# Kernel tuning notes

Measured on AMD Instinct MI355X. Metric: run time of the kernel, lower is better.

Reference implementation:

```python
import jax, jax.numpy as jnp
import numpy as np

B, C, H, W = 512, 1, 280, 280
K, S, F = 28, 28, 10           # kernel, stride, nfilters
HS, WS = 10, 10                # output spatial spans (280/28)
SPAN = HS * WS                 # 100 patch locations
OUT = 10                       # out_channels
DEC_IN = HS * WS * F           # 1000


def setup_inputs() -> dict:
    key = jax.random.key(0)
    k1, k2, k3, k4, k5 = jax.random.split(key, 5)
    x = jax.random.normal(k1, (B, C, H, W), dtype=jnp.float32)
    # locally-connected weights: one kernel per (filter, spatial location), torch layout [F*SPAN, C, K, K]
    conv_w = jax.random.normal(k2, (F * SPAN, C, K, K), dtype=jnp.float32) * 0.02
    conv_b = jax.random.normal(k3, (F * SPAN, C), dtype=jnp.float32) * 0.02
    dec_w = jax.random.normal(k4, (OUT, DEC_IN), dtype=jnp.float32) * 0.02
    dec_b = jax.random.normal(k5, (OUT,), dtype=jnp.float32) * 0.02
    return {"x": x, "conv_w": conv_w, "conv_b": conv_b, "dec_w": dec_w, "dec_b": dec_b}


def reference(x, conv_w, conv_b, dec_w, dec_b):
    # Extract non-overlapping KxK patches (stride == kernel_size, padding == 0):
    # [B,C,H,W] -> [B,C,HS,K,WS,K] -> [B,HS,WS,C,K,K] -> [B,SPAN,C,K,K]
    # matches torch unfold(2).unfold(3) ordering (height span outer, width span inner).
    patches = x.reshape(B, C, HS, K, WS, K).transpose(0, 2, 4, 1, 3, 5)
    patches = patches.reshape(B, SPAN, C, K, K)
    # weight index in torch is f*SPAN + s (x is tiled SPAN-fastest by repeat)
    w = conv_w.reshape(F, SPAN, C, K, K)
    # per-location elementwise mul + reduce over (kh, kw) == batched tiny contraction
    out = jnp.einsum('bscij,fscij->bfsc', patches, w)  # [B,F,SPAN,C]
    out = out + conv_b.reshape(F, SPAN, C)
    out = out.reshape(B, F, HS, WS)  # valid since C == 1 (as in torch view)
    out = jax.nn.relu(out).reshape(B, DEC_IN)
    return out @ dec_w.T + dec_b
```

## Files before the change

### kernel.cpp

```cpp
#include <hip/hip_runtime.h>

#define HW      280
#define IMG     78400
#define KK      28
#define F_N     10
#define SPAN    100
#define OUT_N   10
#define NB      4
#define RQR     7
#define WQ      (RQR * 7)
#define P_PLANE 512000

__device__ __forceinline__ float red8(float v) {
  v += __int_as_float(__builtin_amdgcn_mov_dpp(__float_as_int(v), 0xB1,  0xF, 0xF, true));
  v += __int_as_float(__builtin_amdgcn_mov_dpp(__float_as_int(v), 0x4E,  0xF, 0xF, true));
  v += __int_as_float(__builtin_amdgcn_mov_dpp(__float_as_int(v), 0x141, 0xF, 0xF, true));
  return v;
}

__global__ __launch_bounds__(256, 4) void lcn_conv(
    const float* __restrict__ x, const float* __restrict__ cw,
    float* __restrict__ P) {
  const int bid = blockIdx.x;
  const int xcd = bid & 7;
  const int idx = bid >> 3;
  const int ws  = idx % 10;
  const int u   = xcd * 20 + idx / 10;
  const int hs  = u % 10;
  const int t   = u / 10;
  const int rq  = t >> 2;
  const int bg  = t & 3;
  const int s   = hs * 10 + ws;

  const int lane = threadIdx.x & 63;
  const int wid  = threadIdx.x >> 6;
  const int c4   = lane & 7;
  const int g    = lane >> 3;
  const int b0   = bg * 128 + wid * 32 + g * 4;

  __shared__ float4 wl[F_N * WQ];
  {
    const float4* wg = reinterpret_cast<const float4*>(cw);
    for (int i = (int)threadIdx.x; i < F_N * WQ; i += 256) {
      const int f = i / WQ, rem = i - f * WQ;
      wl[i] = wg[(f * SPAN + s) * 196 + rq * WQ + rem];
    }
  }
  __syncthreads();

  float acc[NB][F_N];
#pragma unroll
  for (int bi = 0; bi < NB; ++bi)
#pragma unroll
    for (int f = 0; f < F_N; ++f) acc[bi][f] = 0.f;

  const float* xb = x + (size_t)(hs * KK + rq * RQR) * HW + ws * KK + c4 * 4;

#define LOADROW(SLOT, ROW)                                                \
  _Pragma("unroll")                                                       \
  for (int bi = 0; bi < NB; ++bi)                                         \
    xv[SLOT][bi] = *reinterpret_cast<const float4*>(                      \
        xb + (size_t)(b0 + bi) * IMG + (size_t)(ROW) * HW);

#define COMPUTE(ROW, SLOT)                                                \
  {                                                                       \
    _Pragma("unroll")                                                     \
    for (int f = 0; f < F_N; ++f) {                                       \
      const float4 wv = wl[f * WQ + (ROW) * 7 + c4];                      \
      _Pragma("unroll")                                                   \
      for (int bi = 0; bi < NB; ++bi) {                                   \
        acc[bi][f] = fmaf(xv[SLOT][bi].x, wv.x, acc[bi][f]);              \
        acc[bi][f] = fmaf(xv[SLOT][bi].y, wv.y, acc[bi][f]);              \
        acc[bi][f] = fmaf(xv[SLOT][bi].z, wv.z, acc[bi][f]);              \
        acc[bi][f] = fmaf(xv[SLOT][bi].w, wv.w, acc[bi][f]);              \
      }                                                                   \
    }                                                                     \
  }

  if (c4 < 7) {
    float4 xv[3][NB];
    LOADROW(0, 0)
    LOADROW(1, 1)
#pragma unroll
    for (int r = 0; r < RQR; ++r) {
      const int slot = r % 3;
      if (r + 2 < RQR) { const int ns = (r + 2) % 3; LOADROW(ns, r + 2) }
      COMPUTE(r, slot)
    }
  }

#pragma unroll
  for (int bi = 0; bi < NB; ++bi)
#pragma unroll
    for (int f = 0; f < F_N; ++f) acc[bi][f] = red8(acc[bi][f]);

  float* Pp = P + (size_t)rq * P_PLANE + (size_t)s * 512 + b0;
#pragma unroll
  for (int f = 0; f < F_N; ++f) {
    if (c4 == f || c4 == f - 8) {
      float4 v4 = make_float4(acc[0][f], acc[1][f], acc[2][f], acc[3][f]);
      *reinterpret_cast<float4*>(&Pp[(size_t)f * (SPAN * 512)]) = v4;
    }
  }
}

__global__ __launch_bounds__(256) void lcn_dec(
    const float* __restrict__ P, const float* __restrict__ cb,
    const float* __restrict__ dw, float* __restrict__ yp) {
  const int bid    = blockIdx.x;
  const int dchunk = bid >> 3;
  const int bg     = bid & 7;
  const int lane   = threadIdx.x & 63;
  const int swid   = __builtin_amdgcn_readfirstlane((int)(threadIdx.x >> 6));
  const int d0     = dchunk * 40 + swid * 10;

  const float* Pb = P + (size_t)bg * 64 + lane;
  float acc[OUT_N];
#pragma unroll
  for (int o = 0; o < OUT_N; ++o) acc[o] = 0.f;

#pragma unroll
  for (int dd = 0; dd < 10; ++dd) {
    const int d = d0 + dd;
    const float* pd = Pb + (size_t)d * 512;
    const float p = pd[0] + pd[P_PLANE] + pd[2 * (size_t)P_PLANE] + pd[3 * (size_t)P_PLANE];
    const float h = fmaxf(p + cb[d], 0.f);
#pragma unroll
    for (int o = 0; o < OUT_N; ++o)
      acc[o] = fmaf(h, dw[o * 1000 + d], acc[o]);
  }
  float* ypp = yp + (size_t)(dchunk * 4 + swid) * 5120 + bg * 64 + lane;
#pragma unroll
  for (int o = 0; o < OUT_N; ++o) ypp[(size_t)o * 512] = acc[o];
}

__global__ __launch_bounds__(256) void lcn_yred(
    const float* __restrict__ yp, const float* __restrict__ db,
    float* __restrict__ y) {
  const int idx = blockIdx.x * 256 + (int)threadIdx.x;
  const int o = idx >> 9;
  const int b = idx & 511;
  float a = db[o];
#pragma unroll 10
  for (int p = 0; p < 100; ++p) a += yp[(size_t)p * 5120 + idx];
  y[b * OUT_N + o] = a;
}

extern "C" void kernel_launch(void* const* d_in, const int* in_sizes, int n_in,
                              void* d_out, int out_size, void* d_ws, size_t ws_size,
                              hipStream_t stream) {
  const float* x  = (const float*)d_in[0];
  const float* cw = (const float*)d_in[1];
  const float* cb = (const float*)d_in[2];
  const float* dw = (const float*)d_in[3];
  const float* db = (const float*)d_in[4];
  float* y = (float*)d_out;

  float* P  = (float*)d_ws;
  float* yp = P + 4 * (size_t)P_PLANE;

  lcn_conv<<<dim3(1600), dim3(256), 0, stream>>>(x, cw, P);
  lcn_dec <<<dim3(200),  dim3(256), 0, stream>>>(P, cb, dw, yp);
  lcn_yred<<<dim3(20),   dim3(256), 0, stream>>>(yp, db, y);
}
```

Before: 45.56 us.

## Rewrite locally-connected conv with bf16 MFMA and LDS double-buffered input rows

Adds a weight-prep kernel that converts conv weights to bf16 in a padded per-row layout. The conv kernel becomes bf16 MFMA 16x16x32 tiles over 16-image batch groups. Input rows are staged through swizzled, double-buffered LDS, with prefetching of the next row overlapped with the MFMAs. This replaces scalar FP32 FMAs and the DPP reductions. In exchange it loses precision (bf16 inputs and weights), adds an extra launch for weight conversion on every call, and pays the cost of converting input to bf16 in LDS.

```diff
diff --git a/kernel.cpp b/kernel.cpp
--- a/kernel.cpp
+++ b/kernel.cpp
@@ -1,4 +1,5 @@
 #include <hip/hip_runtime.h>
+#include <hip/hip_bf16.h>
 
 #define HW      280
 #define IMG     78400
@@ -6,100 +7,130 @@
 #define F_N     10
 #define SPAN    100
 #define OUT_N   10
-#define NB      4
-#define RQR     7
-#define WQ      (RQR * 7)
 #define P_PLANE 512000
 
-__device__ __forceinline__ float red8(float v) {
-  v += __int_as_float(__builtin_amdgcn_mov_dpp(__float_as_int(v), 0xB1,  0xF, 0xF, true));
-  v += __int_as_float(__builtin_amdgcn_mov_dpp(__float_as_int(v), 0x4E,  0xF, 0xF, true));
-  v += __int_as_float(__builtin_amdgcn_mov_dpp(__float_as_int(v), 0x141, 0xF, 0xF, true));
-  return v;
+typedef short s16x8 __attribute__((ext_vector_type(8)));
+typedef float f32x4 __attribute__((ext_vector_type(4)));
+
+__global__ __launch_bounds__(256) void wprep(const float* __restrict__ cw,
+                                             unsigned* __restrict__ wbuf) {
+  const int idx = blockIdx.x * 256 + (int)threadIdx.x;
+  const int k2  = idx & 15;
+  const int f   = (idx >> 4) & 15;
+  const int rs  = idx >> 8;
+  const int r   = rs % 28;
+  const int s   = rs / 28;
+  unsigned out = 0;
+  if (f < F_N) {
+    const int k0 = k2 * 2, k1 = k0 + 1;
+    const float v0 = (k0 < KK) ? cw[(size_t)(f * SPAN + s) * (KK * KK) + r * KK + k0] : 0.f;
+    const float v1 = (k1 < KK) ? cw[(size_t)(f * SPAN + s) * (KK * KK) + r * KK + k1] : 0.f;
+    __hip_bfloat162 h2 = __float22bfloat162_rn(make_float2(v0, v1));
+    out = *reinterpret_cast<unsigned*>(&h2);
+  }
+  wbuf[idx] = out;
 }
 
 __global__ __launch_bounds__(256, 4) void lcn_conv(
-    const float* __restrict__ x, const float* __restrict__ cw,
+    const float* __restrict__ x, const unsigned short* __restrict__ wbuf,
     float* __restrict__ P) {
-  const int bid = blockIdx.x;
-  const int xcd = bid & 7;
-  const int idx = bid >> 3;
-  const int ws  = idx % 10;
-  const int u   = xcd * 20 + idx / 10;
-  const int hs  = u % 10;
-  const int t   = u / 10;
-  const int rq  = t >> 2;
-  const int bg  = t & 3;
-  const int s   = hs * 10 + ws;
+  const int bid  = blockIdx.x;
+  const int xcd  = bid & 7;
+  const int grp  = bid >> 3;
+  const int hsrq = xcd + 8 * (grp % 5);
+  const int bg   = grp / 5;
+  const int hs   = hsrq >> 2;
+  const int rq   = hsrq & 3;
 
-  const int lane = threadIdx.x & 63;
-  const int wid  = threadIdx.x >> 6;
-  const int c4   = lane & 7;
-  const int g    = lane >> 3;
-  const int b0   = bg * 128 + wid * 32 + g * 4;
+  const int tid  = (int)threadIdx.x;
+  const int lane = tid & 63;
+  const int wid  = tid >> 6;
+  const int l15  = lane & 15;
+  const int kg   = lane >> 4;
 
-  __shared__ float4 wl[F_N * WQ];
-  {
-    const float4* wg = reinterpret_cast<const float4*>(cw);
-    for (int i = (int)threadIdx.x; i < F_N * WQ; i += 256) {
-      const int f = i / WQ, rem = i - f * WQ;
-      wl[i] = wg[(f * SPAN + s) * 196 + rq * WQ + rem];
+  __shared__ short xl[2][16 * 320];
+
+  for (int i = tid; i < 2 * 160; i += 256) {
+    const int buf = i / 160, j = i - buf * 160;
+    const int b = j / 10, ws = j - b * 10;
+    const int sidx = (b * 320 + ws * 32 + 28) ^ ((b & 7) << 3);
+    *reinterpret_cast<short4*>(&xl[buf][sidx]) = make_short4(0, 0, 0, 0);
+  }
+
+  const int nun = (wid < 2) ? 3 : 2;
+  const int wsl[3] = {wid, wid + 4, wid + 8};
+
+  f32x4 acc[3];
+#pragma unroll
+  for (int u = 0; u < 3; ++u) acc[u] = (f32x4){0.f, 0.f, 0.f, 0.f};
+
+  const int row0 = hs * KK + rq * 7;
+  const float* xbase = x + (size_t)bg * 16 * IMG + (size_t)row0 * HW;
+
+  float4 stg[5];
+  auto issue = [&](int r) {
+#pragma unroll
+    for (int j = 0; j < 5; ++j) {
+      const int i = tid + 256 * j;
+      if (i < 1120) {
+        const int b = i / 70, q = i - b * 70;
+        stg[j] = *reinterpret_cast<const float4*>(
+            xbase + (size_t)b * IMG + (size_t)r * HW + q * 4);
+      }
     }
-  }
+  };
+  auto commit = [&](int buf) {
+#pragma unroll
+    for (int j = 0; j < 5; ++j) {
+      const int i = tid + 256 * j;
+      if (i < 1120) {
+        const int b = i / 70, q = i - b * 70;
+        const int ws = q / 7, c4 = q - ws * 7;
+        __hip_bfloat162 h0 = __float22bfloat162_rn(make_float2(stg[j].x, stg[j].y));
+        __hip_bfloat162 h1 = __float22bfloat162_rn(make_float2(stg[j].z, stg[j].w));
+        const int sidx = (b * 320 + ws * 32 + c4 * 4) ^ ((b & 7) << 3);
+        uint2 pk;
+        pk.x = *reinterpret_cast<unsigned*>(&h0);
+        pk.y = *reinterpret_cast<unsigned*>(&h1);
+        *reinterpret_cast<uint2*>(&xl[buf][sidx]) = pk;
+      }
+    }
+  };
+
+  issue(0);
+  commit(0);
   __syncthreads();
 
-  float acc[NB][F_N];
+  for (int r = 0; r < 7; ++r) {
+    const int buf = r & 1;
+    if (r < 6) issue(r + 1);
+    const int rr = rq * 7 + r;
 #pragma unroll
-  for (int bi = 0; bi < NB; ++bi)
-#pragma unroll
-    for (int f = 0; f < F_N; ++f) acc[bi][f] = 0.f;
-
-  const float* xb = x + (size_t)(hs * KK + rq * RQR) * HW + ws * KK + c4 * 4;
-
-#define LOADROW(SLOT, ROW)                                                \
-  _Pragma("unroll")                                                       \
-  for (int bi = 0; bi < NB; ++bi)                                         \
-    xv[SLOT][bi] = *reinterpret_cast<const float4*>(                      \
-        xb + (size_t)(b0 + bi) * IMG + (size_t)(ROW) * HW);
-
-#define COMPUTE(ROW, SLOT)                                                \
-  {                                                                       \
-    _Pragma("unroll")                                                     \
-    for (int f = 0; f < F_N; ++f) {                                       \
-      const float4 wv = wl[f * WQ + (ROW) * 7 + c4];                      \
-      _Pragma("unroll")                                                   \
-      for (int bi = 0; bi < NB; ++bi) {                                   \
-        acc[bi][f] = fmaf(xv[SLOT][bi].x, wv.x, acc[bi][f]);              \
-        acc[bi][f] = fmaf(xv[SLOT][bi].y, wv.y, acc[bi][f]);              \
-        acc[bi][f] = fmaf(xv[SLOT][bi].z, wv.z, acc[bi][f]);              \
-        acc[bi][f] = fmaf(xv[SLOT][bi].w, wv.w, acc[bi][f]);              \
-      }                                                                   \
-    }                                                                     \
+    for (int u = 0; u < 3; ++u) {
+      if (u < nun) {
+        const int ws = wsl[u];
+        const int s  = hs * 10 + ws;
+        const s16x8 bfr = *reinterpret_cast<const s16x8*>(
+            wbuf + (size_t)(s * 28 + rr) * 512 + l15 * 32 + kg * 8);
+        const int sidx = (l15 * 320 + ws * 32 + kg * 8) ^ ((l15 & 7) << 3);
+        const s16x8 afr = *reinterpret_cast<const s16x8*>(&xl[buf][sidx]);
+        acc[u] = __builtin_amdgcn_mfma_f32_16x16x32_bf16(afr, bfr, acc[u], 0, 0, 0);
+      }
+    }
+    if (r < 6) commit(buf ^ 1);
+    __syncthreads();
   }
 
-  if (c4 < 7) {
-    float4 xv[3][NB];
-    LOADROW(0, 0)
-    LOADROW(1, 1)
+  if (l15 < F_N) {
 #pragma unroll
-    for (int r = 0; r < RQR; ++r) {
-      const int slot = r % 3;
-      if (r + 2 < RQR) { const int ns = (r + 2) % 3; LOADROW(ns, r + 2) }
-      COMPUTE(r, slot)
-    }
-  }
-
-#pragma unroll
-  for (int bi = 0; bi < NB; ++bi)
-#pragma unroll
-    for (int f = 0; f < F_N; ++f) acc[bi][f] = red8(acc[bi][f]);
-
-  float* Pp = P + (size_t)rq * P_PLANE + (size_t)s * 512 + b0;
-#pragma unroll
-  for (int f = 0; f < F_N; ++f) {
-    if (c4 == f || c4 == f - 8) {
-      float4 v4 = make_float4(acc[0][f], acc[1][f], acc[2][f], acc[3][f]);
-      *reinterpret_cast<float4*>(&Pp[(size_t)f * (SPAN * 512)]) = v4;
+    for (int u = 0; u < 3; ++u) {
+      if (u < nun) {
+        const int s = hs * 10 + wsl[u];
+        float* Pp = P + (size_t)rq * P_PLANE + (size_t)(l15 * SPAN + s) * 512
+                      + bg * 16 + kg * 4;
+        *reinterpret_cast<float4*>(Pp) =
+            make_float4(acc[u][0], acc[u][1], acc[u][2], acc[u][3]);
+      }
     }
   }
 }
@@ -156,10 +187,12 @@
   const float* db = (const float*)d_in[4];
   float* y = (float*)d_out;
 
-  float* P  = (float*)d_ws;
-  float* yp = P + 4 * (size_t)P_PLANE;
+  float*    P    = (float*)d_ws;
+  float*    yp   = P + 4 * (size_t)P_PLANE;
+  unsigned* wbuf = (unsigned*)(yp + 100 * 5120);
 
-  lcn_conv<<<dim3(1600), dim3(256), 0, stream>>>(x, cw, P);
+  wprep   <<<dim3(2800), dim3(256), 0, stream>>>(cw, wbuf);
+  lcn_conv<<<dim3(1280), dim3(256), 0, stream>>>(x, (const unsigned short*)wbuf, P);
   lcn_dec <<<dim3(200),  dim3(256), 0, stream>>>(P, cb, dw, yp);
   lcn_yred<<<dim3(20),   dim3(256), 0, stream>>>(yp, db, y);
 }
```

Result: slower. 47.60 us (+4.5%).
